# Kernel optimization log

Hardware: AMD Instinct MI355X
Metric: run time of the kernel (lower is better)

## Reference

```python
import math
import jax, jax.numpy as jnp
import numpy as np

N, E = 20000, 640000
S_DIM, Z_DIM, H, QK, VD = 64, 64, 4, 8, 8
EPS = 1e-8


def quat_rotate(v, q):
    # v: [..., 3], q: [..., 4] (w, x, y, z), broadcastable. Unit-quaternion rotation:
    # v' = v + 2*(w*(u x v) + u x (u x v))
    w = q[..., 0:1]
    u = q[..., 1:4]
    uv = jnp.cross(u, v)
    return v + 2.0 * (w * uv + jnp.cross(u, uv))


def setup_inputs() -> dict:
    key = jax.random.key(0)
    ks = jax.random.split(key, 16)
    s = jax.random.normal(ks[0], (N, S_DIM), dtype=jnp.float32)
    z = jax.random.normal(ks[1], (E, Z_DIM), dtype=jnp.float32)
    edge_index = jax.random.randint(ks[2], (2, E), 0, N)
    quaternion = jax.random.normal(ks[3], (N, 4), dtype=jnp.float32)
    quaternion = quaternion / jnp.linalg.norm(quaternion, axis=-1, keepdims=True)
    translation = jax.random.normal(ks[4], (N, 3), dtype=jnp.float32)
    sc_s = 1.0 / math.sqrt(S_DIM)
    sc_z = 1.0 / math.sqrt(Z_DIM)
    # weights stored [in, out] so y = x @ W (equivalent to torch x @ W.T)
    Wq_s = jax.random.normal(ks[5], (S_DIM, H * S_DIM), dtype=jnp.float32) * sc_s
    Wk_s = jax.random.normal(ks[6], (S_DIM, H * S_DIM), dtype=jnp.float32) * sc_s
    Wv_s = jax.random.normal(ks[7], (S_DIM, H * S_DIM), dtype=jnp.float32) * sc_s
    Wq_v = jax.random.normal(ks[8], (S_DIM, H * QK * 3), dtype=jnp.float32) * sc_s
    Wk_v = jax.random.normal(ks[9], (S_DIM, H * QK * 3), dtype=jnp.float32) * sc_s
    Wv_v = jax.random.normal(ks[10], (S_DIM, H * VD * 3), dtype=jnp.float32) * sc_s
    Wb = jax.random.normal(ks[11], (Z_DIM, H), dtype=jnp.float32) * sc_z
    bb = jnp.zeros((H,), dtype=jnp.float32)
    Wdz = jax.random.normal(ks[12], (Z_DIM, Z_DIM // 4), dtype=jnp.float32) * sc_z
    bdz = jnp.zeros((Z_DIM // 4,), dtype=jnp.float32)
    head_weights = jnp.full((H,), 0.541324854612918, dtype=jnp.float32)  # softplus^{-1}(1)
    concat_dim = Z_DIM // 4 + S_DIM + VD * 4
    Wout = jax.random.normal(ks[13], (H * concat_dim, S_DIM), dtype=jnp.float32) / math.sqrt(H * concat_dim)
    bout = jnp.zeros((S_DIM,), dtype=jnp.float32)
    return {
        's': s, 'z': z, 'edge_index': edge_index, 'quaternion': quaternion,
        'translation': translation, 'Wq_s': Wq_s, 'Wk_s': Wk_s, 'Wv_s': Wv_s,
        'Wq_v': Wq_v, 'Wk_v': Wk_v, 'Wv_v': Wv_v, 'Wb': Wb, 'bb': bb,
        'Wdz': Wdz, 'bdz': bdz, 'head_weights': head_weights,
        'Wout': Wout, 'bout': bout,
    }


def reference(s, z, edge_index, quaternion, translation,
              Wq_s, Wk_s, Wv_s, Wq_v, Wk_v, Wv_v,
              Wb, bb, Wdz, bdz, head_weights, Wout, bout):
    idx_i, idx_j = edge_index[0], edge_index[1]
    n = s.shape[0]
    h = head_weights.shape[0]
    qk = Wq_v.shape[1] // (3 * h)
    vd = Wv_v.shape[1] // (3 * h)

    q_scalar = (s @ Wq_s).reshape(n, h, -1)
    k_scalar = (s @ Wk_s).reshape(n, h, -1)
    v_scalar = (s @ Wv_s).reshape(n, h, -1)

    def to_points(x):
        # torch.split into 3 chunks then stack(dim=-1): [n, 3*c] -> [n, c, 3]
        c = x.shape[-1] // 3
        return jnp.swapaxes(x.reshape(n, 3, c), 1, 2)

    quat_b = quaternion[:, None, :]
    trans_b = translation[:, None, :]
    q_vec = (quat_rotate(to_points(s @ Wq_v), quat_b) + trans_b).reshape(n, h, qk, 3)
    k_vec = (quat_rotate(to_points(s @ Wk_v), quat_b) + trans_b).reshape(n, h, qk, 3)
    v_vec = (quat_rotate(to_points(s @ Wv_v), quat_b) + trans_b).reshape(n, h, vd, 3)

    b_bias = z @ Wb + bb  # [E, H]

    attn = jnp.sum(k_scalar[idx_i] * q_scalar[idx_j], axis=-1)  # [E, H]
    attn = attn * math.sqrt(1.0 / 3 * qk) + math.sqrt(1.0 / 3) * b_bias

    disp = q_vec[idx_i] - k_vec[idx_j]            # [E, H, qk, 3]
    vec_att = jnp.sum(disp * disp, axis=-1)       # [E, H, qk]
    hw = jax.nn.softplus(head_weights)[None, :, None]
    vec_att = jnp.sum(vec_att * hw, axis=-1) * math.sqrt(1.0 / (3 * (qk * 9.0 / 2))) * (-0.5)
    attn = attn + vec_att

    # segment softmax over destination node idx_i
    seg_max = jax.ops.segment_max(attn, idx_i, num_segments=n)
    ea = jnp.exp(attn - seg_max[idx_i])
    denom = jax.ops.segment_sum(ea, idx_i, num_segments=n)
    attn = ea / denom[idx_i]                      # [E, H]

    out_scalar = jax.ops.segment_sum(attn[:, :, None] * v_scalar[idx_i], idx_i, num_segments=n)
    out_scalar = out_scalar.reshape(n, -1)

    out_vec = jax.ops.segment_sum(attn[:, :, None, None] * v_vec[idx_i], idx_i, num_segments=n)
    out_vec = out_vec - translation[:, None, None, :]
    q_conj = jnp.concatenate([quaternion[:, :1], -quaternion[:, 1:]], axis=-1)
    out_vec = quat_rotate(out_vec, q_conj[:, None, None, :])   # [n, h, vd, 3]
    out_vec_norm = jnp.sqrt(jnp.sum(out_vec * out_vec, axis=-1) + EPS).reshape(n, -1)
    out_vec_flat = out_vec.reshape(n, -1, 3)

    pair_z = z @ Wdz + bdz                         # [E, z/4]
    out_pair = jax.ops.segment_sum(attn[:, :, None] * pair_z[:, None, :], idx_i, num_segments=n)
    out_pair = out_pair.reshape(n, -1)

    feats = jnp.concatenate([out_scalar,
                             out_vec_flat[..., 0], out_vec_flat[..., 1], out_vec_flat[..., 2],
                             out_vec_norm, out_pair], axis=-1)
    return feats @ Wout + bout
```

## Files before the change

### kernel.cpp

```cpp
#include <hip/hip_runtime.h>
#include <stdint.h>


#define C_SQRT83  1.6329931618554518f
#define C_SQRT13  0.5773502691896258f
#define C_VEC    -0.04811252243246881f

__device__ __forceinline__ unsigned short f2bf(float f){
  unsigned u = __float_as_uint(f);
  u += 0x7fffu + ((u >> 16) & 1u);
  return (unsigned short)(u >> 16);
}
__device__ __forceinline__ unsigned pack2(float a, float b){
  return (unsigned)f2bf(a) | ((unsigned)f2bf(b) << 16);
}
__device__ __forceinline__ float bflo(unsigned u){ return __uint_as_float(u << 16); }
__device__ __forceinline__ float bfhi(unsigned u){ return __uint_as_float(u & 0xffff0000u); }

__device__ __forceinline__ void quat_rot(float w, float ux, float uy, float uz,
                                         float vx, float vy, float vz,
                                         float& ox, float& oy, float& oz){
  float cx = uy*vz - uz*vy;
  float cy = uz*vx - ux*vz;
  float cz = ux*vy - uy*vx;
  float dx = uy*cz - uz*cy;
  float dy = uz*cx - ux*cz;
  float dz = ux*cy - uy*cx;
  ox = vx + 2.f*(w*cx + dx);
  oy = vy + 2.f*(w*cy + dy);
  oz = vz + 2.f*(w*cz + dz);
}


__global__ __launch_bounds__(256) void k_count(const int* __restrict__ ei,
                                               unsigned* __restrict__ counts,
                                               unsigned* __restrict__ rank, int ne){
  int e = blockIdx.x*256 + threadIdx.x;
  if (e >= ne) return;
  rank[e] = atomicAdd(&counts[ei[e]], 1u);
}

__global__ __launch_bounds__(256) void k_scan(const unsigned* __restrict__ counts,
                                              unsigned* __restrict__ row_off, int n){
  __shared__ unsigned part[256];
  int t = threadIdx.x;
  int chunk = (n + 255) >> 8;
  int s0 = t*chunk, s1 = min(s0 + chunk, n);
  unsigned sum = 0;
  for (int k = s0; k < s1; ++k) sum += counts[k];
  part[t] = sum; __syncthreads();
  for (int off = 1; off < 256; off <<= 1){
    unsigned v = (t >= off) ? part[t-off] : 0u;
    __syncthreads();
    part[t] += v;
    __syncthreads();
  }
  unsigned run = (t == 0) ? 0u : part[t-1];
  for (int k = s0; k < s1; ++k){
    row_off[k] = run; run += counts[k];
  }
  if (t == 255) row_off[n] = part[255];
}

__global__ __launch_bounds__(256) void k_fill(const int* __restrict__ ei,
                                              const unsigned* __restrict__ rank,
                                              const unsigned* __restrict__ roff,
                                              unsigned* __restrict__ si,
                                              unsigned* __restrict__ sj,
                                              unsigned* __restrict__ se, int ne){
  int e = blockIdx.x*256 + threadIdx.x;
  if (e >= ne) return;
  const int i = ei[e];
  const unsigned pos = roff[i] + rank[e];
  si[pos] = (unsigned)i;
  sj[pos] = (unsigned)ei[ne + e];
  se[pos] = (unsigned)e;
}


#define BN 32

__device__ __forceinline__ void pass256(const float* __restrict__ W,
                                        const float stT[64][40], int cg, int sl,
                                        float acc[8][4]){
  #pragma unroll
  for (int i=0;i<8;i++){ acc[i][0]=0.f; acc[i][1]=0.f; acc[i][2]=0.f; acc[i][3]=0.f; }
  #pragma unroll 4
  for (int k = 0; k < 64; ++k){
    const float4 w  = *(const float4*)(W + (size_t)k*256 + cg*4);
    const float4 n0 = *(const float4*)&stT[k][sl*8];
    const float4 n1 = *(const float4*)&stT[k][sl*8+4];
    acc[0][0]+=n0.x*w.x; acc[0][1]+=n0.x*w.y; acc[0][2]+=n0.x*w.z; acc[0][3]+=n0.x*w.w;
    acc[1][0]+=n0.y*w.x; acc[1][1]+=n0.y*w.y; acc[1][2]+=n0.y*w.z; acc[1][3]+=n0.y*w.w;
    acc[2][0]+=n0.z*w.x; acc[2][1]+=n0.z*w.y; acc[2][2]+=n0.z*w.z; acc[2][3]+=n0.z*w.w;
    acc[3][0]+=n0.w*w.x; acc[3][1]+=n0.w*w.y; acc[3][2]+=n0.w*w.z; acc[3][3]+=n0.w*w.w;
    acc[4][0]+=n1.x*w.x; acc[4][1]+=n1.x*w.y; acc[4][2]+=n1.x*w.z; acc[4][3]+=n1.x*w.w;
    acc[5][0]+=n1.y*w.x; acc[5][1]+=n1.y*w.y; acc[5][2]+=n1.y*w.z; acc[5][3]+=n1.y*w.w;
    acc[6][0]+=n1.z*w.x; acc[6][1]+=n1.z*w.y; acc[6][2]+=n1.z*w.z; acc[6][3]+=n1.z*w.w;
    acc[7][0]+=n1.w*w.x; acc[7][1]+=n1.w*w.y; acc[7][2]+=n1.w*w.z; acc[7][3]+=n1.w*w.w;
  }
}

__device__ __forceinline__ void pass96(const float* __restrict__ W,
                                       const float stT[64][40], int cgp, int slp,
                                       float acc[4][4]){
  #pragma unroll
  for (int i=0;i<4;i++){ acc[i][0]=0.f; acc[i][1]=0.f; acc[i][2]=0.f; acc[i][3]=0.f; }
  if (cgp >= 24) return;
  #pragma unroll 4
  for (int k = 0; k < 64; ++k){
    const float4 w = *(const float4*)(W + (size_t)k*96 + cgp*4);
    const float4 nv = *(const float4*)&stT[k][slp*4];
    acc[0][0]+=nv.x*w.x; acc[0][1]+=nv.x*w.y; acc[0][2]+=nv.x*w.z; acc[0][3]+=nv.x*w.w;
    acc[1][0]+=nv.y*w.x; acc[1][1]+=nv.y*w.y; acc[1][2]+=nv.y*w.z; acc[1][3]+=nv.y*w.w;
    acc[2][0]+=nv.z*w.x; acc[2][1]+=nv.z*w.y; acc[2][2]+=nv.z*w.z; acc[2][3]+=nv.z*w.w;
    acc[3][0]+=nv.w*w.x; acc[3][1]+=nv.w*w.y; acc[3][2]+=nv.w*w.z; acc[3][3]+=nv.w*w.w;
  }
}

__global__ __launch_bounds__(256) void k_proj(
    const float* __restrict__ s, const float* __restrict__ quat, const float* __restrict__ trans,
    const float* __restrict__ Wqs, const float* __restrict__ Wks, const float* __restrict__ Wvs,
    const float* __restrict__ Wqv, const float* __restrict__ Wkv, const float* __restrict__ Wvv,
    unsigned* __restrict__ qs, unsigned* __restrict__ ks, float* __restrict__ vs,
    unsigned* __restrict__ qv, unsigned* __restrict__ kv, float* __restrict__ vv, int n)
{
  __shared__ float stT[64][40];
  __shared__ float pt[BN][97];
  const int tid = threadIdx.x;
  const int node0 = blockIdx.x * BN;

  #pragma unroll
  for (int r = 0; r < 2; ++r){
    const int idx = tid + r*256;
    const int nd = idx >> 4, c4 = idx & 15;
    const int g = node0 + nd;
    float4 v = make_float4(0.f,0.f,0.f,0.f);
    if (g < n) v = *(const float4*)(s + (size_t)g*64 + c4*4);
    stT[c4*4+0][nd]=v.x; stT[c4*4+1][nd]=v.y; stT[c4*4+2][nd]=v.z; stT[c4*4+3][nd]=v.w;
  }
  __syncthreads();

  const int cg = tid & 63, sl = tid >> 6;
  const int cgp = tid & 31, slp = tid >> 5;
  float acc[8][4];

  pass256(Wqs, stT, cg, sl, acc);
  #pragma unroll
  for (int i=0;i<8;i++){
    const int g = node0 + sl*8 + i;
    if (g < n){
      uint2 u; u.x = pack2(acc[i][0],acc[i][1]); u.y = pack2(acc[i][2],acc[i][3]);
      *(uint2*)(qs + (size_t)g*128 + cg*2) = u;
    }
  }
  pass256(Wks, stT, cg, sl, acc);
  #pragma unroll
  for (int i=0;i<8;i++){
    const int g = node0 + sl*8 + i;
    if (g < n){
      uint2 u; u.x = pack2(acc[i][0],acc[i][1]); u.y = pack2(acc[i][2],acc[i][3]);
      *(uint2*)(ks + (size_t)g*128 + cg*2) = u;
    }
  }
  pass256(Wvs, stT, cg, sl, acc);
  #pragma unroll
  for (int i=0;i<8;i++){
    const int g = node0 + sl*8 + i;
    if (g < n){
      float4 f; f.x=acc[i][0]; f.y=acc[i][1]; f.z=acc[i][2]; f.w=acc[i][3];
      *(float4*)(vs + (size_t)g*256 + cg*4) = f;
    }
  }

  float pac[4][4];

  pass96(Wqv, stT, cgp, slp, pac);
  __syncthreads();
  if (cgp < 24){
    #pragma unroll
    for (int i=0;i<4;i++){
      #pragma unroll
      for (int c=0;c<4;c++) pt[slp*4+i][cgp*4+c] = pac[i][c];
    }
  }
  __syncthreads();
  #pragma unroll
  for (int r = 0; r < 2; ++r){
    const int t2 = tid + r*256;
    const int nd = t2 >> 4, pp = t2 & 15;
    const int g = node0 + nd;
    if (g < n){
      const float4 q4 = *(const float4*)(quat + (size_t)g*4);
      const float tx = trans[(size_t)g*3], ty = trans[(size_t)g*3+1], tz = trans[(size_t)g*3+2];
      float x0,y0,z0,x1,y1,z1;
      quat_rot(q4.x,q4.y,q4.z,q4.w, pt[nd][2*pp],   pt[nd][32+2*pp],   pt[nd][64+2*pp],   x0,y0,z0);
      quat_rot(q4.x,q4.y,q4.z,q4.w, pt[nd][2*pp+1], pt[nd][32+2*pp+1], pt[nd][64+2*pp+1], x1,y1,z1);
      x0+=tx; y0+=ty; z0+=tz; x1+=tx; y1+=ty; z1+=tz;
      unsigned* d = qv + (size_t)g*48 + pp*3;
      d[0] = pack2(x0,y0); d[1] = pack2(z0,x1); d[2] = pack2(y1,z1);
    }
  }

  pass96(Wkv, stT, cgp, slp, pac);
  __syncthreads();
  if (cgp < 24){
    #pragma unroll
    for (int i=0;i<4;i++){
      #pragma unroll
      for (int c=0;c<4;c++) pt[slp*4+i][cgp*4+c] = pac[i][c];
    }
  }
  __syncthreads();
  #pragma unroll
  for (int r = 0; r < 2; ++r){
    const int t2 = tid + r*256;
    const int nd = t2 >> 4, pp = t2 & 15;
    const int g = node0 + nd;
    if (g < n){
      const float4 q4 = *(const float4*)(quat + (size_t)g*4);
      const float tx = trans[(size_t)g*3], ty = trans[(size_t)g*3+1], tz = trans[(size_t)g*3+2];
      float x0,y0,z0,x1,y1,z1;
      quat_rot(q4.x,q4.y,q4.z,q4.w, pt[nd][2*pp],   pt[nd][32+2*pp],   pt[nd][64+2*pp],   x0,y0,z0);
      quat_rot(q4.x,q4.y,q4.z,q4.w, pt[nd][2*pp+1], pt[nd][32+2*pp+1], pt[nd][64+2*pp+1], x1,y1,z1);
      x0+=tx; y0+=ty; z0+=tz; x1+=tx; y1+=ty; z1+=tz;
      unsigned* d = kv + (size_t)g*48 + pp*3;
      d[0] = pack2(x0,y0); d[1] = pack2(z0,x1); d[2] = pack2(y1,z1);
    }
  }

  pass96(Wvv, stT, cgp, slp, pac);
  __syncthreads();
  if (cgp < 24){
    #pragma unroll
    for (int i=0;i<4;i++){
      #pragma unroll
      for (int c=0;c<4;c++) pt[slp*4+i][cgp*4+c] = pac[i][c];
    }
  }
  __syncthreads();
  #pragma unroll
  for (int r = 0; r < 12; ++r){
    const int idx = tid + r*256;
    const int nd = idx / 96, col = idx - nd*96;
    const int g = node0 + nd;
    if (g < n) vv[(size_t)g*96 + col] = pt[nd][col];
  }
}


__global__ __launch_bounds__(256) void k_edge(
    const float* __restrict__ z,
    const unsigned* __restrict__ si, const unsigned* __restrict__ sj, const unsigned* __restrict__ se,
    const float* __restrict__ Wb,  const float* __restrict__ bb,
    const float* __restrict__ Wdz, const float* __restrict__ bdz,
    const float* __restrict__ hwts,
    const unsigned* __restrict__ qs, const unsigned* __restrict__ ks,
    const unsigned* __restrict__ qv, const unsigned* __restrict__ kv,
    float* __restrict__ logits, unsigned* __restrict__ pz, int ne)
{
  const int p = blockIdx.x*256 + threadIdx.x;
  if (p >= ne) return;
  const unsigned i = si[p], j = sj[p], e = se[p];

  float b4[4];  b4[0]=b4[1]=b4[2]=b4[3]=0.f;
  float pacc[16];
  #pragma unroll
  for (int c=0;c<16;c++) pacc[c]=0.f;
  const float* zr = z + (size_t)e*64;
  #pragma unroll
  for (int k4 = 0; k4 < 16; ++k4){
    const float4 zv = *(const float4*)(zr + 4*k4);
    #pragma unroll
    for (int kk = 0; kk < 4; ++kk){
      const int k = 4*k4 + kk;
      const float zk = (kk==0)?zv.x:((kk==1)?zv.y:((kk==2)?zv.z:zv.w));
      const float4 wb = *(const float4*)(Wb + k*4);
      b4[0]+=zk*wb.x; b4[1]+=zk*wb.y; b4[2]+=zk*wb.z; b4[3]+=zk*wb.w;
      const float* wd = Wdz + k*16;
      const float4 w0=*(const float4*)(wd), w1=*(const float4*)(wd+4),
                   w2=*(const float4*)(wd+8), w3=*(const float4*)(wd+12);
      pacc[ 0]+=zk*w0.x; pacc[ 1]+=zk*w0.y; pacc[ 2]+=zk*w0.z; pacc[ 3]+=zk*w0.w;
      pacc[ 4]+=zk*w1.x; pacc[ 5]+=zk*w1.y; pacc[ 6]+=zk*w1.z; pacc[ 7]+=zk*w1.w;
      pacc[ 8]+=zk*w2.x; pacc[ 9]+=zk*w2.y; pacc[10]+=zk*w2.z; pacc[11]+=zk*w2.w;
      pacc[12]+=zk*w3.x; pacc[13]+=zk*w3.y; pacc[14]+=zk*w3.z; pacc[15]+=zk*w3.w;
    }
  }
  #pragma unroll
  for (int c=0;c<16;c++) pacc[c] += bdz[c];
  { uint4 u0, u1;
    u0.x=pack2(pacc[0],pacc[1]);   u0.y=pack2(pacc[2],pacc[3]);
    u0.z=pack2(pacc[4],pacc[5]);   u0.w=pack2(pacc[6],pacc[7]);
    u1.x=pack2(pacc[8],pacc[9]);   u1.y=pack2(pacc[10],pacc[11]);
    u1.z=pack2(pacc[12],pacc[13]); u1.w=pack2(pacc[14],pacc[15]);
    uint4* d = (uint4*)(pz + (size_t)p*8);
    d[0]=u0; d[1]=u1; }

  const uint4* kr = (const uint4*)(ks + (size_t)i*128);
  const uint4* qr = (const uint4*)(qs + (size_t)j*128);
  float sdot[4];
  #pragma unroll
  for (int h = 0; h < 4; ++h){
    float acc = 0.f;
    #pragma unroll
    for (int c = 0; c < 8; ++c){
      const uint4 a = kr[h*8+c];
      const uint4 b = qr[h*8+c];
      acc += bflo(a.x)*bflo(b.x) + bfhi(a.x)*bfhi(b.x);
      acc += bflo(a.y)*bflo(b.y) + bfhi(a.y)*bfhi(b.y);
      acc += bflo(a.z)*bflo(b.z) + bfhi(a.z)*bfhi(b.z);
      acc += bflo(a.w)*bflo(b.w) + bfhi(a.w)*bfhi(b.w);
    }
    sdot[h] = acc;
  }

  const uint4* qvr = (const uint4*)(qv + (size_t)i*48);
  const uint4* kvr = (const uint4*)(kv + (size_t)j*48);
  float vsum[4];
  #pragma unroll
  for (int h = 0; h < 4; ++h){
    float acc = 0.f;
    #pragma unroll
    for (int c = 0; c < 3; ++c){
      const uint4 a = qvr[h*3+c];
      const uint4 b = kvr[h*3+c];
      float d;
      d = bflo(a.x)-bflo(b.x); acc += d*d;  d = bfhi(a.x)-bfhi(b.x); acc += d*d;
      d = bflo(a.y)-bflo(b.y); acc += d*d;  d = bfhi(a.y)-bfhi(b.y); acc += d*d;
      d = bflo(a.z)-bflo(b.z); acc += d*d;  d = bfhi(a.z)-bfhi(b.z); acc += d*d;
      d = bflo(a.w)-bflo(b.w); acc += d*d;  d = bfhi(a.w)-bfhi(b.w); acc += d*d;
    }
    vsum[h] = acc;
  }

  float4 lg;
  {
    float l[4];
    #pragma unroll
    for (int h = 0; h < 4; ++h){
      const float hw = log1pf(__expf(hwts[h]));
      l[h] = C_SQRT83*sdot[h] + C_SQRT13*(b4[h] + bb[h]) + C_VEC*hw*vsum[h];
    }
    lg.x=l[0]; lg.y=l[1]; lg.z=l[2]; lg.w=l[3];
  }
  *(float4*)(logits + (size_t)p*4) = lg;
}


__global__ __launch_bounds__(256) void k_soft(
    const float* __restrict__ logits, const unsigned* __restrict__ pz,
    const unsigned* __restrict__ row_off, float* __restrict__ out_pair, int n)
{
  const int node = blockIdx.x*4 + (threadIdx.x >> 6);
  if (node >= n) return;
  const int lane = threadIdx.x & 63;
  const int beg = (int)row_off[node], end = (int)row_off[node+1];

  float m[4] = {-3.0e38f,-3.0e38f,-3.0e38f,-3.0e38f};
  for (int p = beg + lane; p < end; p += 64){
    const float4 l = *(const float4*)(logits + (size_t)p*4);
    m[0]=fmaxf(m[0],l.x); m[1]=fmaxf(m[1],l.y); m[2]=fmaxf(m[2],l.z); m[3]=fmaxf(m[3],l.w);
  }
  #pragma unroll
  for (int msk = 1; msk < 64; msk <<= 1){
    #pragma unroll
    for (int h=0;h<4;h++) m[h] = fmaxf(m[h], __shfl_xor(m[h], msk));
  }
  float S[4] = {0.f,0.f,0.f,0.f};
  for (int p = beg + lane; p < end; p += 64){
    const float4 l = *(const float4*)(logits + (size_t)p*4);
    S[0]+=__expf(l.x-m[0]); S[1]+=__expf(l.y-m[1]);
    S[2]+=__expf(l.z-m[2]); S[3]+=__expf(l.w-m[3]);
  }
  #pragma unroll
  for (int msk = 1; msk < 64; msk <<= 1){
    #pragma unroll
    for (int h=0;h<4;h++) S[h] += __shfl_xor(S[h], msk);
  }
  float inv[4];
  #pragma unroll
  for (int h=0;h<4;h++) inv[h] = (S[h] > 0.f) ? (1.f/S[h]) : 0.f;

  const int e4 = lane >> 4, c = lane & 15;
  float acc[4] = {0.f,0.f,0.f,0.f};
  for (int base = beg; base < end; base += 4){
    const int p = base + e4;
    if (p < end){
      const float4 l = *(const float4*)(logits + (size_t)p*4);
      const unsigned u = pz[(size_t)p*8 + (c>>1)];
      const float pzv = (c & 1) ? bfhi(u) : bflo(u);
      acc[0] += __expf(l.x-m[0]) * pzv;
      acc[1] += __expf(l.y-m[1]) * pzv;
      acc[2] += __expf(l.z-m[2]) * pzv;
      acc[3] += __expf(l.w-m[3]) * pzv;
    }
  }
  #pragma unroll
  for (int msk = 16; msk < 64; msk <<= 1){
    #pragma unroll
    for (int h=0;h<4;h++) acc[h] += __shfl_xor(acc[h], msk);
  }
  const int hOut = lane >> 4;
  out_pair[(size_t)node*64 + lane] = acc[hOut] * inv[hOut];
}


__global__ __launch_bounds__(256) void k_out(
    const float* __restrict__ vs, const float* __restrict__ vv,
    const float* __restrict__ out_pair, const unsigned* __restrict__ row_off,
    const float* __restrict__ quat, const float* __restrict__ trans,
    const float* __restrict__ Wout, const float* __restrict__ bout,
    float* __restrict__ out, int n)
{
  __shared__ float feats[32][448];
  __shared__ int degs[32];
  const int tid = threadIdx.x;
  const int node0 = blockIdx.x*32;

  if (tid < 32){
    const int g = node0 + tid;
    degs[tid] = (g < n) ? (int)(row_off[g+1] - row_off[g]) : 1;
  }
  __syncthreads();

  for (int x = tid; x < 32*256; x += 256){
    const int nd = x >> 8, c = x & 255;
    const int g = node0 + nd;
    feats[nd][c] = (g < n && degs[nd] > 0) ? vs[(size_t)g*256 + c] : 0.f;
  }
  for (int x = tid; x < 32*64; x += 256){
    const int nd = x >> 6, c = x & 63;
    const int g = node0 + nd;
    feats[nd][384 + c] = (g < n) ? out_pair[(size_t)g*64 + c] : 0.f;
  }
  for (int x = tid; x < 32*32; x += 256){
    const int nd = x >> 5, pt = x & 31;
    const int g = node0 + nd;
    float X=0.f, Y=0.f, Z=0.f;
    if (g < n){
      if (degs[nd] > 0){
        X = vv[(size_t)g*96 + pt];
        Y = vv[(size_t)g*96 + 32 + pt];
        Z = vv[(size_t)g*96 + 64 + pt];
      } else {
        const float4 q4 = *(const float4*)(quat + (size_t)g*4);
        const float tx = trans[(size_t)g*3], ty = trans[(size_t)g*3+1], tz = trans[(size_t)g*3+2];
        quat_rot(q4.x, -q4.y, -q4.z, -q4.w, -tx, -ty, -tz, X, Y, Z);
      }
    }
    feats[nd][256 + pt] = X;
    feats[nd][288 + pt] = Y;
    feats[nd][320 + pt] = Z;
    feats[nd][352 + pt] = sqrtf(X*X + Y*Y + Z*Z + 1e-8f);
  }
  __syncthreads();

  const int lane = tid & 63;
  const int wave = tid >> 6;
  float acc[8];
  #pragma unroll
  for (int q8=0;q8<8;q8++) acc[q8]=0.f;

  for (int k0 = 0; k0 < 448; k0 += 4){
    const float w0 = Wout[(size_t)(k0+0)*64 + lane];
    const float w1 = Wout[(size_t)(k0+1)*64 + lane];
    const float w2 = Wout[(size_t)(k0+2)*64 + lane];
    const float w3 = Wout[(size_t)(k0+3)*64 + lane];
    #pragma unroll
    for (int q8 = 0; q8 < 8; ++q8){
      const float4 f = *(const float4*)&feats[wave*8 + q8][k0];
      acc[q8] += f.x*w0 + f.y*w1 + f.z*w2 + f.w*w3;
    }
  }
  const float bo = bout[lane];
  #pragma unroll
  for (int q8 = 0; q8 < 8; ++q8){
    const int g = node0 + wave*8 + q8;
    if (g < n) out[(size_t)g*64 + lane] = acc[q8] + bo;
  }
}


extern "C" void kernel_launch(void* const* d_in, const int* in_sizes, int n_in,
                              void* d_out, int out_size, void* d_ws, size_t ws_size,
                              hipStream_t stream) {
  const float* s     = (const float*)d_in[0];
  const float* z     = (const float*)d_in[1];
  const int*   ei    = (const int*)  d_in[2];
  const float* quat  = (const float*)d_in[3];
  const float* trans = (const float*)d_in[4];
  const float* Wqs   = (const float*)d_in[5];
  const float* Wks   = (const float*)d_in[6];
  const float* Wvs   = (const float*)d_in[7];
  const float* Wqv   = (const float*)d_in[8];
  const float* Wkv   = (const float*)d_in[9];
  const float* Wvv   = (const float*)d_in[10];
  const float* Wb    = (const float*)d_in[11];
  const float* bb    = (const float*)d_in[12];
  const float* Wdz   = (const float*)d_in[13];
  const float* bdz   = (const float*)d_in[14];
  const float* hwts  = (const float*)d_in[15];
  const float* Wout  = (const float*)d_in[16];
  const float* bout  = (const float*)d_in[17];
  float* out = (float*)d_out;

  const int n  = in_sizes[0] / 64;
  const int ne = in_sizes[1] / 64;

  size_t off = 0;
  char* base = (char*)d_ws;
  auto take = [&](size_t bytes)->char* {
    char* p = base + off;
    off += (bytes + 255) & ~(size_t)255;
    return p;
  };
  unsigned* qs     = (unsigned*)take((size_t)n*512);
  unsigned* ks     = (unsigned*)take((size_t)n*512);
  unsigned* qvt    = (unsigned*)take((size_t)n*192);
  unsigned* kvt    = (unsigned*)take((size_t)n*192);
  float*    vs     = (float*)   take((size_t)n*1024);
  float*    vv     = (float*)   take((size_t)n*384);
  float*    logits = (float*)   take((size_t)ne*16);
  unsigned* pz     = (unsigned*)take((size_t)ne*32);
  unsigned* counts = (unsigned*)take((size_t)n*4);
  unsigned* roff   = (unsigned*)take((size_t)(n+1)*4);
  unsigned* rank   = (unsigned*)take((size_t)ne*4);
  unsigned* si     = (unsigned*)take((size_t)ne*4);
  unsigned* sj     = (unsigned*)take((size_t)ne*4);
  unsigned* se     = (unsigned*)take((size_t)ne*4);
  float*    opair  = (float*)   take((size_t)n*256);
  (void)ws_size; (void)n_in; (void)out_size;

  const int gbE = (ne + 255) / 256;

  hipMemsetAsync(counts, 0, (size_t)n*4, stream);
  k_count<<<gbE, 256, 0, stream>>>(ei, counts, rank, ne);
  k_scan <<<1,   256, 0, stream>>>(counts, roff, n);
  k_fill <<<gbE, 256, 0, stream>>>(ei, rank, roff, si, sj, se, ne);
  k_proj <<<(n + BN - 1)/BN, 256, 0, stream>>>(s, quat, trans, Wqs, Wks, Wvs, Wqv, Wkv, Wvv,
                                               qs, ks, vs, qvt, kvt, vv, n);
  k_edge <<<gbE, 256, 0, stream>>>(z, si, sj, se, Wb, bb, Wdz, bdz, hwts,
                                   qs, ks, qvt, kvt, logits, pz, ne);
  k_soft <<<(n + 3)/4, 256, 0, stream>>>(logits, pz, roff, opair, n);
  k_out  <<<(n + 31)/32, 256, 0, stream>>>(vs, vv, opair, roff, quat, trans,
                                           Wout, bout, out, n);
}
```

Before: 655.1 us.

## Move z-projection into fill kernel to read z coalesced in edge order

The per-edge z projections (bias logits and the pair_z features) now run in the fill kernel. That kernel iterates edges in original order, so z is read coalesced, and it scatters the results to sorted positions. This replaces the gather of z rows through the permutation array in k_edge and removes the se array. The cost is that k_edge must read the bias back from the logits buffer, and the fill kernel's writes become scattered.

```diff
diff --git a/kernel.cpp b/kernel.cpp
--- a/kernel.cpp
+++ b/kernel.cpp
@@ -62,19 +62,61 @@
   if (t == 255) row_off[n] = part[255];
 }
 
-__global__ __launch_bounds__(256) void k_fill(const int* __restrict__ ei,
-                                              const unsigned* __restrict__ rank,
-                                              const unsigned* __restrict__ roff,
-                                              unsigned* __restrict__ si,
-                                              unsigned* __restrict__ sj,
-                                              unsigned* __restrict__ se, int ne){
-  int e = blockIdx.x*256 + threadIdx.x;
+
+__global__ __launch_bounds__(256) void k_zfill(
+    const int* __restrict__ ei, const unsigned* __restrict__ rank,
+    const unsigned* __restrict__ roff, const float* __restrict__ z,
+    const float* __restrict__ Wb,  const float* __restrict__ bb,
+    const float* __restrict__ Wdz, const float* __restrict__ bdz,
+    unsigned* __restrict__ si, unsigned* __restrict__ sj,
+    float* __restrict__ logits, unsigned* __restrict__ pz, int ne)
+{
+  const int e = blockIdx.x*256 + threadIdx.x;
   if (e >= ne) return;
   const int i = ei[e];
   const unsigned pos = roff[i] + rank[e];
   si[pos] = (unsigned)i;
   sj[pos] = (unsigned)ei[ne + e];
-  se[pos] = (unsigned)e;
+
+  float b4[4];  b4[0]=b4[1]=b4[2]=b4[3]=0.f;
+  float pacc[16];
+  #pragma unroll
+  for (int c=0;c<16;c++) pacc[c]=0.f;
+  const float* zr = z + (size_t)e*64;
+  #pragma unroll
+  for (int k4 = 0; k4 < 16; ++k4){
+    const float4 zv = *(const float4*)(zr + 4*k4);
+    #pragma unroll
+    for (int kk = 0; kk < 4; ++kk){
+      const int k = 4*k4 + kk;
+      const float zk = (kk==0)?zv.x:((kk==1)?zv.y:((kk==2)?zv.z:zv.w));
+      const float4 wb = *(const float4*)(Wb + k*4);
+      b4[0]+=zk*wb.x; b4[1]+=zk*wb.y; b4[2]+=zk*wb.z; b4[3]+=zk*wb.w;
+      const float* wd = Wdz + k*16;
+      const float4 w0=*(const float4*)(wd), w1=*(const float4*)(wd+4),
+                   w2=*(const float4*)(wd+8), w3=*(const float4*)(wd+12);
+      pacc[ 0]+=zk*w0.x; pacc[ 1]+=zk*w0.y; pacc[ 2]+=zk*w0.z; pacc[ 3]+=zk*w0.w;
+      pacc[ 4]+=zk*w1.x; pacc[ 5]+=zk*w1.y; pacc[ 6]+=zk*w1.z; pacc[ 7]+=zk*w1.w;
+      pacc[ 8]+=zk*w2.x; pacc[ 9]+=zk*w2.y; pacc[10]+=zk*w2.z; pacc[11]+=zk*w2.w;
+      pacc[12]+=zk*w3.x; pacc[13]+=zk*w3.y; pacc[14]+=zk*w3.z; pacc[15]+=zk*w3.w;
+    }
+  }
+  #pragma unroll
+  for (int c=0;c<16;c++) pacc[c] += bdz[c];
+  { uint4 u0, u1;
+    u0.x=pack2(pacc[0],pacc[1]);   u0.y=pack2(pacc[2],pacc[3]);
+    u0.z=pack2(pacc[4],pacc[5]);   u0.w=pack2(pacc[6],pacc[7]);
+    u1.x=pack2(pacc[8],pacc[9]);   u1.y=pack2(pacc[10],pacc[11]);
+    u1.z=pack2(pacc[12],pacc[13]); u1.w=pack2(pacc[14],pacc[15]);
+    uint4* d = (uint4*)(pz + (size_t)pos*8);
+    d[0]=u0; d[1]=u1; }
+
+  float4 bo;
+  bo.x = C_SQRT13*(b4[0] + bb[0]);
+  bo.y = C_SQRT13*(b4[1] + bb[1]);
+  bo.z = C_SQRT13*(b4[2] + bb[2]);
+  bo.w = C_SQRT13*(b4[3] + bb[3]);
+  *(float4*)(logits + (size_t)pos*4) = bo;
 }
 
 
@@ -250,51 +292,17 @@
 
 
 __global__ __launch_bounds__(256) void k_edge(
-    const float* __restrict__ z,
-    const unsigned* __restrict__ si, const unsigned* __restrict__ sj, const unsigned* __restrict__ se,
-    const float* __restrict__ Wb,  const float* __restrict__ bb,
-    const float* __restrict__ Wdz, const float* __restrict__ bdz,
+    const unsigned* __restrict__ si, const unsigned* __restrict__ sj,
     const float* __restrict__ hwts,
     const unsigned* __restrict__ qs, const unsigned* __restrict__ ks,
     const unsigned* __restrict__ qv, const unsigned* __restrict__ kv,
-    float* __restrict__ logits, unsigned* __restrict__ pz, int ne)
+    float* __restrict__ logits, int ne)
 {
   const int p = blockIdx.x*256 + threadIdx.x;
   if (p >= ne) return;
-  const unsigned i = si[p], j = sj[p], e = se[p];
-
-  float b4[4];  b4[0]=b4[1]=b4[2]=b4[3]=0.f;
-  float pacc[16];
-  #pragma unroll
-  for (int c=0;c<16;c++) pacc[c]=0.f;
-  const float* zr = z + (size_t)e*64;
-  #pragma unroll
-  for (int k4 = 0; k4 < 16; ++k4){
-    const float4 zv = *(const float4*)(zr + 4*k4);
-    #pragma unroll
-    for (int kk = 0; kk < 4; ++kk){
-      const int k = 4*k4 + kk;
-      const float zk = (kk==0)?zv.x:((kk==1)?zv.y:((kk==2)?zv.z:zv.w));
-      const float4 wb = *(const float4*)(Wb + k*4);
-      b4[0]+=zk*wb.x; b4[1]+=zk*wb.y; b4[2]+=zk*wb.z; b4[3]+=zk*wb.w;
-      const float* wd = Wdz + k*16;
-      const float4 w0=*(const float4*)(wd), w1=*(const float4*)(wd+4),
-                   w2=*(const float4*)(wd+8), w3=*(const float4*)(wd+12);
-      pacc[ 0]+=zk*w0.x; pacc[ 1]+=zk*w0.y; pacc[ 2]+=zk*w0.z; pacc[ 3]+=zk*w0.w;
-      pacc[ 4]+=zk*w1.x; pacc[ 5]+=zk*w1.y; pacc[ 6]+=zk*w1.z; pacc[ 7]+=zk*w1.w;
-      pacc[ 8]+=zk*w2.x; pacc[ 9]+=zk*w2.y; pacc[10]+=zk*w2.z; pacc[11]+=zk*w2.w;
-      pacc[12]+=zk*w3.x; pacc[13]+=zk*w3.y; pacc[14]+=zk*w3.z; pacc[15]+=zk*w3.w;
-    }
-  }
-  #pragma unroll
-  for (int c=0;c<16;c++) pacc[c] += bdz[c];
-  { uint4 u0, u1;
-    u0.x=pack2(pacc[0],pacc[1]);   u0.y=pack2(pacc[2],pacc[3]);
-    u0.z=pack2(pacc[4],pacc[5]);   u0.w=pack2(pacc[6],pacc[7]);
-    u1.x=pack2(pacc[8],pacc[9]);   u1.y=pack2(pacc[10],pacc[11]);
-    u1.z=pack2(pacc[12],pacc[13]); u1.w=pack2(pacc[14],pacc[15]);
-    uint4* d = (uint4*)(pz + (size_t)p*8);
-    d[0]=u0; d[1]=u1; }
+  const unsigned i = si[p], j = sj[p];
+
+  const float4 bias = *(const float4*)(logits + (size_t)p*4);
 
   const uint4* kr = (const uint4*)(ks + (size_t)i*128);
   const uint4* qr = (const uint4*)(qs + (size_t)j*128);
@@ -336,10 +344,12 @@
   float4 lg;
   {
     float l[4];
+    const float4 b4 = bias;
+    const float bb4[4] = {b4.x, b4.y, b4.z, b4.w};
     #pragma unroll
     for (int h = 0; h < 4; ++h){
       const float hw = log1pf(__expf(hwts[h]));
-      l[h] = C_SQRT83*sdot[h] + C_SQRT13*(b4[h] + bb[h]) + C_VEC*hw*vsum[h];
+      l[h] = C_SQRT83*sdot[h] + bb4[h] + C_VEC*hw*vsum[h];
     }
     lg.x=l[0]; lg.y=l[1]; lg.z=l[2]; lg.w=l[3];
   }
@@ -527,7 +537,6 @@
   unsigned* rank   = (unsigned*)take((size_t)ne*4);
   unsigned* si     = (unsigned*)take((size_t)ne*4);
   unsigned* sj     = (unsigned*)take((size_t)ne*4);
-  unsigned* se     = (unsigned*)take((size_t)ne*4);
   float*    opair  = (float*)   take((size_t)n*256);
   (void)ws_size; (void)n_in; (void)out_size;
 
@@ -536,11 +545,11 @@
   hipMemsetAsync(counts, 0, (size_t)n*4, stream);
   k_count<<<gbE, 256, 0, stream>>>(ei, counts, rank, ne);
   k_scan <<<1,   256, 0, stream>>>(counts, roff, n);
-  k_fill <<<gbE, 256, 0, stream>>>(ei, rank, roff, si, sj, se, ne);
+  k_zfill<<<gbE, 256, 0, stream>>>(ei, rank, roff, z, Wb, bb, Wdz, bdz,
+                                   si, sj, logits, pz, ne);
   k_proj <<<(n + BN - 1)/BN, 256, 0, stream>>>(s, quat, trans, Wqs, Wks, Wvs, Wqv, Wkv, Wvv,
                                                qs, ks, vs, qvt, kvt, vv, n);
-  k_edge <<<gbE, 256, 0, stream>>>(z, si, sj, se, Wb, bb, Wdz, bdz, hwts,
-                                   qs, ks, qvt, kvt, logits, pz, ne);
+  k_edge <<<gbE, 256, 0, stream>>>(si, sj, hwts, qs, ks, qvt, kvt, logits, ne);
   k_soft <<<(n + 3)/4, 256, 0, stream>>>(logits, pz, roff, opair, n);
   k_out  <<<(n + 31)/32, 256, 0, stream>>>(vs, vv, opair, roff, quat, trans,
                                            Wout, bout, out, n);
```

After: 702.1 us. 7.2% more time.
